# Optimization experiments

Hardware: AMD Instinct MI355X
Metric: run time of the kernel (lower is better)

Reference implementation:

```python
import jax, jax.numpy as jnp
import numpy as np

A = 81          # agents / zones (9x9 grid)
DMAX = 5        # max neighborhood size (self + 4-neighbors)
NGLOB = 48      # global obs block width
HID = 128
B = 16384
LN_EPS = 1e-12  # tf.contrib.layers.layer_norm epsilon
BN_EPS = 1e-3   # tf.contrib.layers.batch_norm epsilon
NEG = -1e30


def _grid_adjacency():
    side = 9
    idx = np.zeros((A, DMAX), np.int32)
    mask = np.zeros((A, DMAX), bool)
    for i in range(A):
        r, c = divmod(i, side)
        nb = [i]
        for dr, dc in ((-1, 0), (1, 0), (0, -1), (0, 1)):
            rr, cc = r + dr, c + dc
            if 0 <= rr < side and 0 <= cc < side:
                nb.append(rr * side + cc)
        idx[i, :len(nb)] = nb
        mask[i, :len(nb)] = True
    return jnp.asarray(idx), jnp.asarray(mask)


def setup_inputs() -> dict:
    key = jax.random.key(0)
    ks = jax.random.split(key, 8)
    neigh_idx, neigh_mask = _grid_adjacency()
    in_dim = 2 * DMAX + NGLOB  # padded local obs width (58)
    s = 0.05
    return {
        "obs": jax.random.normal(ks[0], (B, 210), jnp.float32),
        "neigh_idx": neigh_idx,
        "neigh_mask": neigh_mask,
        "W1": jax.random.normal(ks[1], (A, in_dim, HID), jnp.float32) * s,
        "b1": jnp.zeros((A, HID), jnp.float32),
        "ln1_g": jnp.ones((A, HID), jnp.float32),
        "ln1_b": jnp.zeros((A, HID), jnp.float32),
        "bn1_b": jnp.zeros((A, HID), jnp.float32),
        "W2": jax.random.normal(ks[2], (A, HID, HID), jnp.float32) * s,
        "b2": jnp.zeros((A, HID), jnp.float32),
        "ln2_g": jnp.ones((A, HID), jnp.float32),
        "ln2_b": jnp.zeros((A, HID), jnp.float32),
        "bn2_b": jnp.zeros((A, HID), jnp.float32),
        "Wout": jax.random.normal(ks[3], (A, HID, DMAX), jnp.float32) * s,
        "bout": jnp.zeros((A, DMAX), jnp.float32),
    }


def _layer_norm(x, g, b):
    mu = jnp.mean(x, axis=-1, keepdims=True)
    var = jnp.mean(jnp.square(x - mu), axis=-1, keepdims=True)
    return (x - mu) * jax.lax.rsqrt(var + LN_EPS) * g[:, None, :] + b[:, None, :]


def _batch_norm(x, beta):
    # training-mode batch norm over the batch axis (axis=1), center only (scale=False)
    mu = jnp.mean(x, axis=1, keepdims=True)
    var = jnp.mean(jnp.square(x - mu), axis=1, keepdims=True)
    return (x - mu) * jax.lax.rsqrt(var + BN_EPS) + beta[:, None, :]


def reference(obs, neigh_idx, neigh_mask, W1, b1, ln1_g, ln1_b, bn1_b,
              W2, b2, ln2_g, ln2_b, bn2_b, Wout, bout):
    m = neigh_mask[:, None, :].astype(obs.dtype)          # [A,1,DMAX]
    g1 = obs[:, NGLOB + neigh_idx].transpose(1, 0, 2)      # [A,B,DMAX] zone block 1
    g2 = obs[:, NGLOB + 81 + neigh_idx].transpose(1, 0, 2)  # [A,B,DMAX] zone block 2
    glob = jnp.broadcast_to(obs[None, :, :NGLOB], (A, obs.shape[0], NGLOB))
    x = jnp.concatenate([g1 * m, g2 * m, glob], axis=-1)   # [A,B,58] (padded slots zeroed)

    h = jnp.einsum('abi,aio->abo', x, W1) + b1[:, None, :]
    h = jax.nn.relu(_batch_norm(_layer_norm(h, ln1_g, ln1_b), bn1_b))
    h = jnp.einsum('abi,aio->abo', h, W2) + b2[:, None, :]
    h = jax.nn.relu(_batch_norm(_layer_norm(h, ln2_g, ln2_b), bn2_b))

    logits = jnp.einsum('abi,aid->abd', h, Wout) + bout[:, None, :]  # [A,B,DMAX]
    logits = jnp.where(neigh_mask[:, None, :], logits, NEG)
    p = jax.nn.softmax(logits, axis=-1) * m                # masked softmax over valid neighbors

    oh = jax.nn.one_hot(neigh_idx, A, dtype=p.dtype)       # [A,DMAX,81] scatter map
    out = jnp.einsum('abd,adn->abn', p, oh)                # scatter into fixed 81-vector
    return out.transpose(1, 0, 2)                          # [B,A,81]
```

## Files before the change

### kernel.cpp

```cpp
#include <hip/hip_runtime.h>
#include <stdint.h>
#include <stddef.h>

#define N_AG 81
#define HID 128
#define TROWS 128

typedef __bf16 bf16x8 __attribute__((ext_vector_type(8)));
typedef float f32x4 __attribute__((ext_vector_type(4)));
typedef uint32_t u32v4 __attribute__((ext_vector_type(4)));
typedef uint32_t u32v2 __attribute__((ext_vector_type(2)));

#define PB1 0
#define PLG1 128
#define PLB1 256
#define PBN1 384
#define PMU1 512
#define PRS1 640
#define PB2 768
#define PLG2 896
#define PLB2 1024
#define PBN2 1152
#define PMU2 1280
#define PRS2 1408

__device__ __forceinline__ unsigned short f2bf(float f) {
  uint32_t u = __builtin_bit_cast(uint32_t, f);
  u += 0x7fffu + ((u >> 16) & 1u);
  return (unsigned short)(u >> 16);
}

__device__ __forceinline__ f32x4 f4z() { f32x4 v; v[0]=0.f; v[1]=0.f; v[2]=0.f; v[3]=0.f; return v; }

__device__ __forceinline__ bf16x8 ld_frag(const uint8_t* p) {
  u32v4 v = *(const u32v4*)p;
  return __builtin_bit_cast(bf16x8, v);
}

__device__ __forceinline__ f32x4 mfma16(bf16x8 a, bf16x8 b, f32x4 c) {
  return __builtin_amdgcn_mfma_f32_16x16x32_bf16(a, b, c, 0, 0, 0);
}

__device__ __forceinline__ void bias_ln(f32x4 (&acc)[8][2], const float* s_par,
                                        int PB, int PG, int PBb, int g) {
  #pragma unroll
  for (int mf = 0; mf < 8; ++mf) {
    #pragma unroll
    for (int rg = 0; rg < 4; ++rg) {
      float bo = s_par[PB + 16 * mf + 4 * g + rg];
      acc[mf][0][rg] += bo;
      acc[mf][1][rg] += bo;
    }
  }
  #pragma unroll
  for (int nf = 0; nf < 2; ++nf) {
    float s = 0.f;
    #pragma unroll
    for (int mf = 0; mf < 8; ++mf) {
      #pragma unroll
      for (int rg = 0; rg < 4; ++rg) s += acc[mf][nf][rg];
    }
    s += __shfl_xor(s, 16);
    s += __shfl_xor(s, 32);
    float mu = s * (1.f / 128.f);
    float qs = 0.f;
    #pragma unroll
    for (int mf = 0; mf < 8; ++mf) {
      #pragma unroll
      for (int rg = 0; rg < 4; ++rg) { float d = acc[mf][nf][rg] - mu; qs += d * d; }
    }
    qs += __shfl_xor(qs, 16);
    qs += __shfl_xor(qs, 32);
    float rstd = rsqrtf(qs * (1.f / 128.f) + 1e-12f);
    #pragma unroll
    for (int mf = 0; mf < 8; ++mf) {
      #pragma unroll
      for (int rg = 0; rg < 4; ++rg) {
        int o = 16 * mf + 4 * g + rg;
        acc[mf][nf][rg] = (acc[mf][nf][rg] - mu) * rstd * s_par[PG + o] + s_par[PBb + o];
      }
    }
  }
}

__device__ __forceinline__ void stats_wave(const f32x4 (&acc)[8][2],
                                           float (&s_red)[2][4][128],
                                           int wv, int g, int q) {
  #pragma unroll
  for (int mf = 0; mf < 8; ++mf) {
    #pragma unroll
    for (int rg = 0; rg < 4; ++rg) {
      float s = acc[mf][0][rg] + acc[mf][1][rg];
      float qq = acc[mf][0][rg] * acc[mf][0][rg] + acc[mf][1][rg] * acc[mf][1][rg];
      s += __shfl_xor(s, 1); s += __shfl_xor(s, 2); s += __shfl_xor(s, 4); s += __shfl_xor(s, 8);
      qq += __shfl_xor(qq, 1); qq += __shfl_xor(qq, 2); qq += __shfl_xor(qq, 4); qq += __shfl_xor(qq, 8);
      if (q == 0) {
        int o = 16 * mf + 4 * g + rg;
        s_red[0][wv][o] = s;
        s_red[1][wv][o] = qq;
      }
    }
  }
}

__global__ void prep_weights(const float* __restrict__ W1, const float* __restrict__ W2,
                             uint8_t* __restrict__ w1img, uint8_t* __restrict__ w2img) {
  const int a = blockIdx.x, t = threadIdx.x;
  for (int i = t; i < 128 * 64; i += 256) {
    int o = i & 127, kk = i >> 7;
    float v = (kk < 58) ? W1[((size_t)a * 58 + kk) * 128 + o] : 0.f;
    uint32_t cb = 2u * kk;
    uint32_t phys = o * 128 + (((cb & ~15u) ^ (((uint32_t)o & 7u) << 4)) | (cb & 15u));
    *(unsigned short*)(w1img + (size_t)a * 16384 + phys) = f2bf(v);
  }
  for (int i = t; i < 128 * 128; i += 256) {
    int o = i & 127, kk = i >> 7;
    float v = W2[((size_t)a * 128 + kk) * 128 + o];
    uint32_t cb = 2u * kk;
    uint32_t phys = o * 256 + (((cb & ~15u) ^ (((uint32_t)o & 7u) << 4)) | (cb & 15u));
    *(unsigned short*)(w2img + (size_t)a * 32768 + phys) = f2bf(v);
  }
}

__global__ void reduce_stats(const float* __restrict__ partS, const float* __restrict__ partQ,
                             float* __restrict__ mu, float* __restrict__ rs) {
  const int a = blockIdx.x, c = threadIdx.x;
  float S = 0.f, Q = 0.f;
  for (int tb = 0; tb < 32; ++tb) {
    S += partS[((size_t)a * 32 + tb) * HID + c];
    Q += partQ[((size_t)a * 32 + tb) * HID + c];
  }
  float m = S * (1.f / 16384.f);
  float v = Q * (1.f / 16384.f) - m * m;
  mu[a * HID + c] = m;
  rs[a * HID + c] = rsqrtf(v + 1e-3f);
}

template <int PASS>
__launch_bounds__(256, 2)
__global__ void pass_kernel(
    const float* __restrict__ obs, const int* __restrict__ nidx,
    const float* __restrict__ b1, const float* __restrict__ ln1g,
    const float* __restrict__ ln1b, const float* __restrict__ bnb1,
    const float* __restrict__ b2, const float* __restrict__ ln2g,
    const float* __restrict__ ln2b, const float* __restrict__ bnb2,
    const float* __restrict__ wout, const float* __restrict__ boutp,
    const uint8_t* __restrict__ w1img, const uint8_t* __restrict__ w2img,
    const float* __restrict__ mu1, const float* __restrict__ rs1,
    const float* __restrict__ mu2, const float* __restrict__ rs2,
    float* __restrict__ partS, float* __restrict__ partQ,
    float* __restrict__ out) {
  __shared__ __align__(16) uint8_t s_main[49152];
  __shared__ float s_par[12 * 128];
  __shared__ float s_wout[HID * 5];
  __shared__ float s_bout[8];
  __shared__ float s_red[2][4][128];

  const int t = threadIdx.x;
  const int wv = t >> 6, l = t & 63, g = l >> 4, q = l & 15;

  int a, sub, tile0, ntl;
  if constexpr (PASS == 3) {
    a = blockIdx.x >> 7; tile0 = blockIdx.x & 127; sub = 0; ntl = 1;
  } else {
    a = blockIdx.x >> 5; sub = blockIdx.x & 31; tile0 = sub * 4; ntl = 4;
  }

  const int r9 = a / 9, c9 = a - 9 * r9;
  const int deg = 1 + (r9 > 0) + (r9 < 8) + (c9 > 0) + (c9 < 8);
  int nid[5];
  #pragma unroll
  for (int d = 0; d < 5; ++d) nid[d] = nidx[a * 5 + d];

  if (t < HID) {
    s_par[PB1 + t] = b1[a * HID + t];
    s_par[PLG1 + t] = ln1g[a * HID + t];
    s_par[PLB1 + t] = ln1b[a * HID + t];
    if constexpr (PASS >= 2) {
      s_par[PBN1 + t] = bnb1[a * HID + t];
      s_par[PMU1 + t] = mu1[a * HID + t];
      s_par[PRS1 + t] = rs1[a * HID + t];
      s_par[PB2 + t] = b2[a * HID + t];
      s_par[PLG2 + t] = ln2g[a * HID + t];
      s_par[PLB2 + t] = ln2b[a * HID + t];
    }
    if constexpr (PASS == 3) {
      s_par[PBN2 + t] = bnb2[a * HID + t];
      s_par[PMU2 + t] = mu2[a * HID + t];
      s_par[PRS2 + t] = rs2[a * HID + t];
      #pragma unroll
      for (int d = 0; d < 5; ++d) s_wout[t * 5 + d] = wout[(a * HID + t) * 5 + d];
    }
  }
  if constexpr (PASS == 3) {
    if (t < 5) s_bout[t] = boutp[a * 5 + t];
  }

  float Sacc = 0.f, Qacc = 0.f;
  const uint8_t* w1src = w1img + (size_t)a * 16384;
  const uint8_t* w2src = w2img + (size_t)a * 32768;

  for (int tt = 0; tt < ntl; ++tt) {
    const int tile = tile0 + tt;

    if (PASS != 1 || tt == 0) {
      #pragma unroll
      for (int i = 0; i < 4; ++i) {
        int idx = t + 256 * i;
        ((u32v4*)(s_main + 16384))[idx] = ((const u32v4*)w1src)[idx];
      }
    }
    if constexpr (PASS >= 2) {
      #pragma unroll
      for (int i = 0; i < 4; ++i) {
        int idx = t + 256 * i;
        int row = idx >> 3, ch = idx & 7;
        *(u32v4*)(s_main + 32768 + row * 128 + ch * 16) =
            *(const u32v4*)(w2src + row * 256 + ch * 16);
      }
    }
    {
      const int xr = t >> 1, xh = t & 1;
      const int bg = tile * TROWS + xr;
      const float* orow = obs + (size_t)bg * 210;
      #pragma unroll
      for (int jj = 0; jj < 4; ++jj) {
        unsigned short us[8];
        #pragma unroll
        for (int e = 0; e < 8; ++e) {
          const int k = 32 * xh + 8 * jj + e;
          float v;
          if (k < 5)       v = (k < deg) ? orow[48 + nid[k]] : 0.f;
          else if (k < 10) v = ((k - 5) < deg) ? orow[129 + nid[k - 5]] : 0.f;
          else if (k < 58) v = orow[k - 10];
          else             v = 0.f;
          us[e] = f2bf(v);
        }
        u32v4 pk;
        pk[0] = (uint32_t)us[0] | ((uint32_t)us[1] << 16);
        pk[1] = (uint32_t)us[2] | ((uint32_t)us[3] << 16);
        pk[2] = (uint32_t)us[4] | ((uint32_t)us[5] << 16);
        pk[3] = (uint32_t)us[6] | ((uint32_t)us[7] << 16);
        uint32_t cb = ((uint32_t)(16 * (4 * xh + jj))) ^ (((uint32_t)xr & 7u) << 4);
        *(u32v4*)(s_main + xr * 128 + cb) = pk;
      }
    }
    __syncthreads();

    f32x4 acc1[8][2];
    #pragma unroll
    for (int mf = 0; mf < 8; ++mf) { acc1[mf][0] = f4z(); acc1[mf][1] = f4z(); }
    {
      const uint8_t* sx = s_main;
      const uint8_t* sw1 = s_main + 16384;
      const int rb = 32 * wv;
      #pragma unroll
      for (int ks = 0; ks < 2; ++ks) {
        bf16x8 bfr[2];
        #pragma unroll
        for (int nf = 0; nf < 2; ++nf) {
          uint32_t r = rb + 16 * nf + q;
          uint32_t cb = ((uint32_t)(64 * ks + 16 * g)) ^ ((r & 7u) << 4);
          bfr[nf] = ld_frag(sx + r * 128 + cb);
        }
        #pragma unroll
        for (int mf = 0; mf < 8; ++mf) {
          uint32_t r = 16 * mf + q;
          uint32_t cb = ((uint32_t)(64 * ks + 16 * g)) ^ ((r & 7u) << 4);
          bf16x8 af = ld_frag(sw1 + r * 128 + cb);
          acc1[mf][0] = mfma16(af, bfr[0], acc1[mf][0]);
          acc1[mf][1] = mfma16(af, bfr[1], acc1[mf][1]);
        }
      }
    }

    bias_ln(acc1, s_par, PB1, PLG1, PLB1, g);

    if constexpr (PASS == 1) {
      stats_wave(acc1, s_red, wv, g, q);
      __syncthreads();
      if (t < HID) {
        Sacc += s_red[0][0][t] + s_red[0][1][t] + s_red[0][2][t] + s_red[0][3][t];
        Qacc += s_red[1][0][t] + s_red[1][1][t] + s_red[1][2][t] + s_red[1][3][t];
      }
    } else {
      __syncthreads();
      #pragma unroll
      for (int mf = 0; mf < 8; ++mf) {
        #pragma unroll
        for (int nf = 0; nf < 2; ++nf) {
          unsigned short us[4];
          #pragma unroll
          for (int rg = 0; rg < 4; ++rg) {
            int o = 16 * mf + 4 * g + rg;
            float z = (acc1[mf][nf][rg] - s_par[PMU1 + o]) * s_par[PRS1 + o] + s_par[PBN1 + o];
            us[rg] = f2bf(fmaxf(z, 0.f));
          }
          uint32_t b_ = 32 * wv + 16 * nf + q;
          uint32_t cb = 2u * (16 * mf + 4 * g);
          uint32_t phys = b_ * 256 + (((cb & ~15u) ^ ((b_ & 7u) << 4)) | (cb & 15u));
          u32v2 pk;
          pk[0] = (uint32_t)us[0] | ((uint32_t)us[1] << 16);
          pk[1] = (uint32_t)us[2] | ((uint32_t)us[3] << 16);
          *(u32v2*)(s_main + phys) = pk;
        }
      }
      __syncthreads();

      f32x4 acc2[8][2];
      #pragma unroll
      for (int mf = 0; mf < 8; ++mf) { acc2[mf][0] = f4z(); acc2[mf][1] = f4z(); }
      {
        const uint8_t* sh1 = s_main;
        const uint8_t* sw2 = s_main + 32768;
        #pragma unroll
        for (int kh = 0; kh < 2; ++kh) {
          if (kh == 1) {
            __syncthreads();
            #pragma unroll
            for (int i = 0; i < 4; ++i) {
              int idx = t + 256 * i;
              int row = idx >> 3, ch = idx & 7;
              *(u32v4*)(s_main + 32768 + row * 128 + ch * 16) =
                  *(const u32v4*)(w2src + row * 256 + 128 + ch * 16);
            }
            __syncthreads();
          }
          #pragma unroll
          for (int kss = 0; kss < 2; ++kss) {
            bf16x8 bfr[2];
            #pragma unroll
            for (int nf = 0; nf < 2; ++nf) {
              uint32_t r = 32 * wv + 16 * nf + q;
              uint32_t cb = ((uint32_t)(128 * kh + 64 * kss + 16 * g)) ^ ((r & 7u) << 4);
              bfr[nf] = ld_frag(sh1 + r * 256 + cb);
            }
            #pragma unroll
            for (int mf = 0; mf < 8; ++mf) {
              uint32_t r = 16 * mf + q;
              uint32_t cb = ((uint32_t)(64 * kss + 16 * g)) ^ ((r & 7u) << 4);
              bf16x8 af = ld_frag(sw2 + r * 128 + cb);
              acc2[mf][0] = mfma16(af, bfr[0], acc2[mf][0]);
              acc2[mf][1] = mfma16(af, bfr[1], acc2[mf][1]);
            }
          }
        }
      }

      bias_ln(acc2, s_par, PB2, PLG2, PLB2, g);

      if constexpr (PASS == 2) {
        stats_wave(acc2, s_red, wv, g, q);
        __syncthreads();
        if (t < HID) {
          Sacc += s_red[0][0][t] + s_red[0][1][t] + s_red[0][2][t] + s_red[0][3][t];
          Qacc += s_red[1][0][t] + s_red[1][1][t] + s_red[1][2][t] + s_red[1][3][t];
        }
      }

      if constexpr (PASS == 3) {
        float lg[2][5];
        #pragma unroll
        for (int nf = 0; nf < 2; ++nf) {
          #pragma unroll
          for (int d = 0; d < 5; ++d) lg[nf][d] = 0.f;
        }
        #pragma unroll
        for (int mf = 0; mf < 8; ++mf) {
          #pragma unroll
          for (int rg = 0; rg < 4; ++rg) {
            int o = 16 * mf + 4 * g + rg;
            float m2 = s_par[PMU2 + o], r2 = s_par[PRS2 + o], bb2 = s_par[PBN2 + o];
            float h0 = fmaxf((acc2[mf][0][rg] - m2) * r2 + bb2, 0.f);
            float h1v = fmaxf((acc2[mf][1][rg] - m2) * r2 + bb2, 0.f);
            #pragma unroll
            for (int d = 0; d < 5; ++d) {
              float wvv = s_wout[o * 5 + d];
              lg[0][d] += h0 * wvv;
              lg[1][d] += h1v * wvv;
            }
          }
        }
        #pragma unroll
        for (int nf = 0; nf < 2; ++nf) {
          #pragma unroll
          for (int d = 0; d < 5; ++d) {
            float v = lg[nf][d];
            v += __shfl_xor(v, 16);
            v += __shfl_xor(v, 32);
            lg[nf][d] = v + s_bout[d];
          }
        }
        float p[2][5];
        #pragma unroll
        for (int nf = 0; nf < 2; ++nf) {
          float mx = lg[nf][0];
          #pragma unroll
          for (int d = 1; d < 5; ++d)
            if (d < deg) mx = fmaxf(mx, lg[nf][d]);
          float den = 0.f;
          #pragma unroll
          for (int d = 0; d < 5; ++d) {
            float e = (d < deg) ? __expf(lg[nf][d] - mx) : 0.f;
            p[nf][d] = e;
            den += e;
          }
          float inv = 1.f / den;
          #pragma unroll
          for (int d = 0; d < 5; ++d) p[nf][d] *= inv;
        }

        __syncthreads();
        float* s_out = (float*)s_main;
        #pragma unroll
        for (int i = 0; i < 11; ++i) {
          int idx = t + 256 * i;
          if (idx < 2688) {
            u32v4 z; z[0] = 0u; z[1] = 0u; z[2] = 0u; z[3] = 0u;
            ((u32v4*)s_out)[idx] = z;
          }
        }
        __syncthreads();
        #pragma unroll
        for (int d = 0; d < 5; ++d) {
          bool writer = (d < 4) ? (g == d) : (g == 0);
          if (writer && d < deg) {
            s_out[(32 * wv + q) * 84 + nid[d]] = p[0][d];
            s_out[(32 * wv + 16 + q) * 84 + nid[d]] = p[1][d];
          }
        }
        __syncthreads();
        const size_t obase = (size_t)(tile * TROWS) * 6561 + (size_t)a * 81;
        for (int i = t; i < 128 * 81; i += 256) {
          int r = i / 81;
          int n = i - r * 81;
          out[obase + (size_t)r * 6561 + n] = s_out[r * 84 + n];
        }
      }
    }
  }

  if constexpr (PASS != 3) {
    if (t < HID) {
      partS[((size_t)a * 32 + sub) * HID + t] = Sacc;
      partQ[((size_t)a * 32 + sub) * HID + t] = Qacc;
    }
  }
}

extern "C" void kernel_launch(void* const* d_in, const int* in_sizes, int n_in,
                              void* d_out, int out_size, void* d_ws, size_t ws_size,
                              hipStream_t stream) {
  const float* obs = (const float*)d_in[0];
  const int* nidx = (const int*)d_in[1];
  const float* W1 = (const float*)d_in[3];
  const float* b1 = (const float*)d_in[4];
  const float* ln1g = (const float*)d_in[5];
  const float* ln1b = (const float*)d_in[6];
  const float* bnb1 = (const float*)d_in[7];
  const float* W2 = (const float*)d_in[8];
  const float* b2 = (const float*)d_in[9];
  const float* ln2g = (const float*)d_in[10];
  const float* ln2b = (const float*)d_in[11];
  const float* bnb2 = (const float*)d_in[12];
  const float* Wout = (const float*)d_in[13];
  const float* bout = (const float*)d_in[14];
  float* out = (float*)d_out;
  uint8_t* ws = (uint8_t*)d_ws;

  uint8_t* w1img = ws;
  uint8_t* w2img = ws + 1327104;
  float* partS1 = (float*)(ws + 3981312);
  float* partQ1 = (float*)(ws + 5308416);
  float* partS2 = (float*)(ws + 6635520);
  float* partQ2 = (float*)(ws + 7962624);
  float* mu1 = (float*)(ws + 9289728);
  float* rs1 = (float*)(ws + 9331200);
  float* mu2 = (float*)(ws + 9372672);
  float* rs2 = (float*)(ws + 9414144);

  prep_weights<<<N_AG, 256, 0, stream>>>(W1, W2, w1img, w2img);

  pass_kernel<1><<<N_AG * 32, 256, 0, stream>>>(
      obs, nidx, b1, ln1g, ln1b, bnb1, b2, ln2g, ln2b, bnb2, Wout, bout,
      w1img, w2img, mu1, rs1, mu2, rs2, partS1, partQ1, out);
  reduce_stats<<<N_AG, 128, 0, stream>>>(partS1, partQ1, mu1, rs1);

  pass_kernel<2><<<N_AG * 32, 256, 0, stream>>>(
      obs, nidx, b1, ln1g, ln1b, bnb1, b2, ln2g, ln2b, bnb2, Wout, bout,
      w1img, w2img, mu1, rs1, mu2, rs2, partS2, partQ2, out);
  reduce_stats<<<N_AG, 128, 0, stream>>>(partS2, partQ2, mu2, rs2);

  pass_kernel<3><<<N_AG * 128, 256, 0, stream>>>(
      obs, nidx, b1, ln1g, ln1b, bnb1, b2, ln2g, ln2b, bnb2, Wout, bout,
      w1img, w2img, mu1, rs1, mu2, rs2, partS1, partQ1, out);
}
```

Measured before the change: 890.9 us.

## Pre-pack global obs to bf16, keep full W2 resident, loop 4 tiles in pass 3

Adds a prep_obs kernel that converts the shared 48-wide global observation block to bf16 once, so each pass copies it into shared memory with vector loads instead of rebuilding it from fp32 for every agent. W1 rows are permuted to match the new column order. W2 is now held whole in a 64KB shared buffer and loaded once per block in pass 2, which removes the mid-loop reload and its barriers. Pass 3 is restructured to process 4 tiles per block, and pass 1 raises its occupancy bound. The cost is the larger shared footprint for passes 2 and 3, plus an extra kernel and workspace region.

```diff
diff --git a/kernel.cpp b/kernel.cpp
--- a/kernel.cpp
+++ b/kernel.cpp
@@ -108,7 +108,10 @@
   const int a = blockIdx.x, t = threadIdx.x;
   for (int i = t; i < 128 * 64; i += 256) {
     int o = i & 127, kk = i >> 7;
-    float v = (kk < 58) ? W1[((size_t)a * 58 + kk) * 128 + o] : 0.f;
+    float v;
+    if (kk < 48)      v = W1[((size_t)a * 58 + (10 + kk)) * 128 + o];
+    else if (kk < 58) v = W1[((size_t)a * 58 + (kk - 48)) * 128 + o];
+    else              v = 0.f;
     uint32_t cb = 2u * kk;
     uint32_t phys = o * 128 + (((cb & ~15u) ^ (((uint32_t)o & 7u) << 4)) | (cb & 15u));
     *(unsigned short*)(w1img + (size_t)a * 16384 + phys) = f2bf(v);
@@ -119,6 +122,24 @@
     uint32_t cb = 2u * kk;
     uint32_t phys = o * 256 + (((cb & ~15u) ^ (((uint32_t)o & 7u) << 4)) | (cb & 15u));
     *(unsigned short*)(w2img + (size_t)a * 32768 + phys) = f2bf(v);
+  }
+}
+
+__global__ void prep_obs(const float* __restrict__ obs, uint8_t* __restrict__ globimg) {
+  const int row = blockIdx.x * 256 + threadIdx.x;
+  if (row >= 16384) return;
+  const float* orow = obs + (size_t)row * 210;
+  uint8_t* dst = globimg + (size_t)row * 96;
+  #pragma unroll
+  for (int c = 0; c < 6; ++c) {
+    u32v4 pk;
+    #pragma unroll
+    for (int e = 0; e < 4; ++e) {
+      float va = orow[8 * c + 2 * e];
+      float vb = orow[8 * c + 2 * e + 1];
+      pk[e] = (uint32_t)f2bf(va) | ((uint32_t)f2bf(vb) << 16);
+    }
+    *(u32v4*)(dst + 16 * c) = pk;
   }
 }
 
@@ -137,7 +158,7 @@
 }
 
 template <int PASS>
-__launch_bounds__(256, 2)
+__launch_bounds__(256, (PASS == 1) ? 4 : 2)
 __global__ void pass_kernel(
     const float* __restrict__ obs, const int* __restrict__ nidx,
     const float* __restrict__ b1, const float* __restrict__ ln1g,
@@ -146,25 +167,25 @@
     const float* __restrict__ ln2b, const float* __restrict__ bnb2,
     const float* __restrict__ wout, const float* __restrict__ boutp,
     const uint8_t* __restrict__ w1img, const uint8_t* __restrict__ w2img,
+    const uint8_t* __restrict__ globimg,
     const float* __restrict__ mu1, const float* __restrict__ rs1,
     const float* __restrict__ mu2, const float* __restrict__ rs2,
     float* __restrict__ partS, float* __restrict__ partQ,
     float* __restrict__ out) {
-  __shared__ __align__(16) uint8_t s_main[49152];
-  __shared__ float s_par[12 * 128];
-  __shared__ float s_wout[HID * 5];
+  constexpr int MAINSZ = (PASS == 1) ? 32768 : 65536;
+  constexpr int PARSZ = (PASS == 1) ? 384 : 1536;
+  __shared__ __align__(16) uint8_t s_main[MAINSZ];
+  __shared__ float s_par[PARSZ];
+  __shared__ float s_red[2][4][128];
+  __shared__ float s_wout[(PASS == 3) ? 640 : 4];
   __shared__ float s_bout[8];
-  __shared__ float s_red[2][4][128];
 
   const int t = threadIdx.x;
   const int wv = t >> 6, l = t & 63, g = l >> 4, q = l & 15;
 
-  int a, sub, tile0, ntl;
-  if constexpr (PASS == 3) {
-    a = blockIdx.x >> 7; tile0 = blockIdx.x & 127; sub = 0; ntl = 1;
-  } else {
-    a = blockIdx.x >> 5; sub = blockIdx.x & 31; tile0 = sub * 4; ntl = 4;
-  }
+  const int a = blockIdx.x >> 5;
+  const int sub = blockIdx.x & 31;
+  const int tile0 = sub * 4;
 
   const int r9 = a / 9, c9 = a - 9 * r9;
   const int deg = 1 + (r9 > 0) + (r9 < 8) + (c9 > 0) + (c9 < 8);
@@ -200,9 +221,19 @@
   const uint8_t* w1src = w1img + (size_t)a * 16384;
   const uint8_t* w2src = w2img + (size_t)a * 32768;
 
-  for (int tt = 0; tt < ntl; ++tt) {
+  for (int tt = 0; tt < 4; ++tt) {
     const int tile = tile0 + tt;
 
+    {
+      const uint8_t* src = globimg + (size_t)tile * (128 * 96);
+      #pragma unroll
+      for (int j = 0; j < 3; ++j) {
+        int u = 3 * t + j;
+        int r = u / 6, c = u - 6 * r;
+        u32v4 v = *(const u32v4*)(src + (size_t)u * 16);
+        *(u32v4*)(s_main + r * 128 + (((uint32_t)c ^ ((uint32_t)r & 7u)) << 4)) = v;
+      }
+    }
     if (PASS != 1 || tt == 0) {
       #pragma unroll
       for (int i = 0; i < 4; ++i) {
@@ -211,39 +242,32 @@
       }
     }
     if constexpr (PASS >= 2) {
-      #pragma unroll
-      for (int i = 0; i < 4; ++i) {
-        int idx = t + 256 * i;
-        int row = idx >> 3, ch = idx & 7;
-        *(u32v4*)(s_main + 32768 + row * 128 + ch * 16) =
-            *(const u32v4*)(w2src + row * 256 + ch * 16);
-      }
-    }
-    {
-      const int xr = t >> 1, xh = t & 1;
-      const int bg = tile * TROWS + xr;
-      const float* orow = obs + (size_t)bg * 210;
-      #pragma unroll
-      for (int jj = 0; jj < 4; ++jj) {
-        unsigned short us[8];
-        #pragma unroll
-        for (int e = 0; e < 8; ++e) {
-          const int k = 32 * xh + 8 * jj + e;
-          float v;
-          if (k < 5)       v = (k < deg) ? orow[48 + nid[k]] : 0.f;
-          else if (k < 10) v = ((k - 5) < deg) ? orow[129 + nid[k - 5]] : 0.f;
-          else if (k < 58) v = orow[k - 10];
-          else             v = 0.f;
-          us[e] = f2bf(v);
-        }
-        u32v4 pk;
-        pk[0] = (uint32_t)us[0] | ((uint32_t)us[1] << 16);
-        pk[1] = (uint32_t)us[2] | ((uint32_t)us[3] << 16);
-        pk[2] = (uint32_t)us[4] | ((uint32_t)us[5] << 16);
-        pk[3] = (uint32_t)us[6] | ((uint32_t)us[7] << 16);
-        uint32_t cb = ((uint32_t)(16 * (4 * xh + jj))) ^ (((uint32_t)xr & 7u) << 4);
-        *(u32v4*)(s_main + xr * 128 + cb) = pk;
-      }
+      if (PASS == 3 || tt == 0) {
+        #pragma unroll
+        for (int i = 0; i < 8; ++i) {
+          int idx = t + 256 * i;
+          ((u32v4*)(s_main + 32768))[idx] = ((const u32v4*)w2src)[idx];
+        }
+      }
+    }
+    if (t < 128) {
+      const int r = t;
+      const float* orow = obs + (size_t)(tile * TROWS + r) * 210;
+      unsigned short us[10];
+      #pragma unroll
+      for (int d = 0; d < 5; ++d) {
+        us[d] = (d < deg) ? f2bf(orow[48 + nid[d]]) : (unsigned short)0;
+        us[5 + d] = (d < deg) ? f2bf(orow[129 + nid[d]]) : (unsigned short)0;
+      }
+      u32v4 c6, c7;
+      c6[0] = (uint32_t)us[0] | ((uint32_t)us[1] << 16);
+      c6[1] = (uint32_t)us[2] | ((uint32_t)us[3] << 16);
+      c6[2] = (uint32_t)us[4] | ((uint32_t)us[5] << 16);
+      c6[3] = (uint32_t)us[6] | ((uint32_t)us[7] << 16);
+      c7[0] = (uint32_t)us[8] | ((uint32_t)us[9] << 16);
+      c7[1] = 0u; c7[2] = 0u; c7[3] = 0u;
+      *(u32v4*)(s_main + r * 128 + ((6u ^ ((uint32_t)r & 7u)) << 4)) = c6;
+      *(u32v4*)(s_main + r * 128 + ((7u ^ ((uint32_t)r & 7u)) << 4)) = c7;
     }
     __syncthreads();
 
@@ -314,35 +338,21 @@
         const uint8_t* sh1 = s_main;
         const uint8_t* sw2 = s_main + 32768;
         #pragma unroll
-        for (int kh = 0; kh < 2; ++kh) {
-          if (kh == 1) {
-            __syncthreads();
-            #pragma unroll
-            for (int i = 0; i < 4; ++i) {
-              int idx = t + 256 * i;
-              int row = idx >> 3, ch = idx & 7;
-              *(u32v4*)(s_main + 32768 + row * 128 + ch * 16) =
-                  *(const u32v4*)(w2src + row * 256 + 128 + ch * 16);
-            }
-            __syncthreads();
-          }
-          #pragma unroll
-          for (int kss = 0; kss < 2; ++kss) {
-            bf16x8 bfr[2];
-            #pragma unroll
-            for (int nf = 0; nf < 2; ++nf) {
-              uint32_t r = 32 * wv + 16 * nf + q;
-              uint32_t cb = ((uint32_t)(128 * kh + 64 * kss + 16 * g)) ^ ((r & 7u) << 4);
-              bfr[nf] = ld_frag(sh1 + r * 256 + cb);
-            }
-            #pragma unroll
-            for (int mf = 0; mf < 8; ++mf) {
-              uint32_t r = 16 * mf + q;
-              uint32_t cb = ((uint32_t)(64 * kss + 16 * g)) ^ ((r & 7u) << 4);
-              bf16x8 af = ld_frag(sw2 + r * 128 + cb);
-              acc2[mf][0] = mfma16(af, bfr[0], acc2[mf][0]);
-              acc2[mf][1] = mfma16(af, bfr[1], acc2[mf][1]);
-            }
+        for (int ks2 = 0; ks2 < 4; ++ks2) {
+          bf16x8 bfr[2];
+          #pragma unroll
+          for (int nf = 0; nf < 2; ++nf) {
+            uint32_t r = 32 * wv + 16 * nf + q;
+            uint32_t cb = ((uint32_t)(64 * ks2 + 16 * g)) ^ ((r & 7u) << 4);
+            bfr[nf] = ld_frag(sh1 + r * 256 + cb);
+          }
+          #pragma unroll
+          for (int mf = 0; mf < 8; ++mf) {
+            uint32_t r = 16 * mf + q;
+            uint32_t cb = ((uint32_t)(64 * ks2 + 16 * g)) ^ ((r & 7u) << 4);
+            bf16x8 af = ld_frag(sw2 + r * 256 + cb);
+            acc2[mf][0] = mfma16(af, bfr[0], acc2[mf][0]);
+            acc2[mf][1] = mfma16(af, bfr[1], acc2[mf][1]);
           }
         }
       }
@@ -436,6 +446,7 @@
           int n = i - r * 81;
           out[obase + (size_t)r * 6561 + n] = s_out[r * 84 + n];
         }
+        __syncthreads();
       }
     }
   }
@@ -470,28 +481,30 @@
 
   uint8_t* w1img = ws;
   uint8_t* w2img = ws + 1327104;
-  float* partS1 = (float*)(ws + 3981312);
-  float* partQ1 = (float*)(ws + 5308416);
-  float* partS2 = (float*)(ws + 6635520);
-  float* partQ2 = (float*)(ws + 7962624);
-  float* mu1 = (float*)(ws + 9289728);
-  float* rs1 = (float*)(ws + 9331200);
-  float* mu2 = (float*)(ws + 9372672);
-  float* rs2 = (float*)(ws + 9414144);
+  uint8_t* globimg = ws + 3981312;
+  float* partS1 = (float*)(ws + 5554176);
+  float* partQ1 = (float*)(ws + 6881280);
+  float* partS2 = (float*)(ws + 8208384);
+  float* partQ2 = (float*)(ws + 9535488);
+  float* mu1 = (float*)(ws + 10862592);
+  float* rs1 = (float*)(ws + 10904064);
+  float* mu2 = (float*)(ws + 10945536);
+  float* rs2 = (float*)(ws + 10987008);
 
   prep_weights<<<N_AG, 256, 0, stream>>>(W1, W2, w1img, w2img);
+  prep_obs<<<64, 256, 0, stream>>>(obs, globimg);
 
   pass_kernel<1><<<N_AG * 32, 256, 0, stream>>>(
       obs, nidx, b1, ln1g, ln1b, bnb1, b2, ln2g, ln2b, bnb2, Wout, bout,
-      w1img, w2img, mu1, rs1, mu2, rs2, partS1, partQ1, out);
+      w1img, w2img, globimg, mu1, rs1, mu2, rs2, partS1, partQ1, out);
   reduce_stats<<<N_AG, 128, 0, stream>>>(partS1, partQ1, mu1, rs1);
 
   pass_kernel<2><<<N_AG * 32, 256, 0, stream>>>(
       obs, nidx, b1, ln1g, ln1b, bnb1, b2, ln2g, ln2b, bnb2, Wout, bout,
-      w1img, w2img, mu1, rs1, mu2, rs2, partS2, partQ2, out);
+      w1img, w2img, globimg, mu1, rs1, mu2, rs2, partS2, partQ2, out);
   reduce_stats<<<N_AG, 128, 0, stream>>>(partS2, partQ2, mu2, rs2);
 
-  pass_kernel<3><<<N_AG * 128, 256, 0, stream>>>(
+  pass_kernel<3><<<N_AG * 32, 256, 0, stream>>>(
       obs, nidx, b1, ln1g, ln1b, bnb1, b2, ln2g, ln2b, bnb2, Wout, bout,
-      w1img, w2img, mu1, rs1, mu2, rs2, partS1, partQ1, out);
-}
+      w1img, w2img, globimg, mu1, rs1, mu2, rs2, partS1, partQ1, out);
+}
```

Result: no change. 891.2 us (+0.0%).
